# Performance work log

Hardware: AMD Instinct MI355X
Metric: run time of the kernel (lower is better)

## Reference

```python
import jax, jax.numpy as jnp
import numpy as np

B, L, D, H, FF = 2, 2048, 1024, 16, 4096


def _xavier(key, out_d, in_d):
    lim = (6.0 / (in_d + out_d)) ** 0.5
    return jax.random.uniform(key, (out_d, in_d), jnp.float32, -lim, lim)


def setup_inputs() -> dict:
    key = jax.random.key(0)
    ks = jax.random.split(key, 7)
    x = jax.random.normal(ks[0], (B, L, D), dtype=jnp.float32)
    wq = _xavier(ks[1], D, D)
    wk = _xavier(ks[2], D, D)
    wv = _xavier(ks[3], D, D)
    wo = _xavier(ks[4], D, D)
    w1 = _xavier(ks[5], FF, D)
    w2 = _xavier(ks[6], D, FF)
    zD = jnp.zeros((D,), jnp.float32)
    return dict(x=x, wq=wq, bq=zD, wk=wk, bk=zD, wv=wv, bv=zD, wo=wo, bo=zD,
                w1=w1, b1=jnp.zeros((FF,), jnp.float32), w2=w2, b2=zD)


def _ln2d(x, eps=1e-5):
    # F.layer_norm(x, x.shape[1:]): normalize jointly over (L, D), no affine
    mu = jnp.mean(x, axis=(1, 2), keepdims=True)
    var = jnp.var(x, axis=(1, 2), keepdims=True)
    return (x - mu) * jax.lax.rsqrt(var + eps)


def reference(x, wq, bq, wk, bk, wv, bv, wo, bo, w1, b1, w2, b2):
    Bx, Lx, Dx = x.shape
    nH = H
    Dh = Dx // nH
    h = _ln2d(x)
    q = (h @ wq.T + bq).reshape(Bx, Lx, nH, Dh).transpose(0, 2, 1, 3)  # (B,H,L,Dh)
    k = (h @ wk.T + bk).reshape(Bx, Lx, nH, Dh).transpose(0, 2, 1, 3)
    v = (h @ wv.T + bv).reshape(Bx, Lx, nH, Dh).transpose(0, 2, 1, 3)
    # NOTE: faithful to source bug: scale = 1/sqrt(key.size(dim=1)) = 1/sqrt(num_heads)
    scale = 1.0 / jnp.sqrt(jnp.asarray(nH, jnp.float32))
    att = jax.nn.softmax(jnp.einsum('bhqd,bhkd->bhqk', q, k) * scale, axis=-1)
    o = jnp.einsum('bhqk,bhkd->bhqd', att, v).transpose(0, 2, 1, 3).reshape(Bx, Lx, Dx)
    o = o @ wo.T + bo
    y = _ln2d(o + x)
    ff = jax.nn.relu(y @ w1.T + b1) @ w2.T + b2
    return ff + x  # second residual adds the ORIGINAL x (as in source)
```

## Files before the change

kernel.cpp:

```cpp
#include <hip/hip_runtime.h>
#include <cstdint>
#include <cstddef>

typedef unsigned short u16;
typedef unsigned int uint;
typedef __bf16 bf16x8 __attribute__((ext_vector_type(8)));
typedef float f32x4 __attribute__((ext_vector_type(4)));

#define BATCH 2
#define SEQ 2048
#define DIM 1024
#define NH 16
#define DH 64
#define FFD 4096
#define MROWS 4096
#define PER_BATCH 2097152

__device__ __forceinline__ u16 f2b(float f) {
  uint u = __builtin_bit_cast(uint, f);
  u += 0x7FFFu + ((u >> 16) & 1u);
  return (u16)(u >> 16);
}

__device__ __forceinline__ uint pkbf2(float a, float b) {
  u16 x = __builtin_bit_cast(u16, (__bf16)a);
  u16 y = __builtin_bit_cast(u16, (__bf16)b);
  return (uint)x | ((uint)y << 16);
}

__device__ __forceinline__ int xcd_swz(int flat, int nwg) {
  return (flat & 7) * (nwg >> 3) + (flat >> 3);
}

#define GLL(gp, lp)                                                            \
  __builtin_amdgcn_global_load_lds(                                            \
      (const __attribute__((address_space(1))) void*)(gp),                     \
      (__attribute__((address_space(3))) void*)(lp), 16, 0, 0)

__global__ __launch_bounds__(256) void cvt4_kernel(const float* __restrict__ s0,
                                                   const float* __restrict__ s1,
                                                   const float* __restrict__ s2,
                                                   const float* __restrict__ s3,
                                                   u16* d0, u16* d1, u16* d2, u16* d3,
                                                   int n) {
  int t = blockIdx.y;
  const float* src = (t == 0) ? s0 : (t == 1) ? s1 : (t == 2) ? s2 : s3;
  u16* dst = (t == 0) ? d0 : (t == 1) ? d1 : (t == 2) ? d2 : d3;
  int i = (blockIdx.x * 256 + threadIdx.x) * 8;
  if (i >= n) return;
  float4 a = *(const float4*)(src + i);
  float4 b = *(const float4*)(src + i + 4);
  uint4 o;
  o.x = f2b(a.x) | ((uint)f2b(a.y) << 16);
  o.y = f2b(a.z) | ((uint)f2b(a.w) << 16);
  o.z = f2b(b.x) | ((uint)f2b(b.y) << 16);
  o.w = f2b(b.z) | ((uint)f2b(b.w) << 16);
  *(uint4*)(dst + i) = o;
}

__global__ __launch_bounds__(256) void reduce_stats_kernel(const float* __restrict__ x,
                                                           float* __restrict__ stats) {
  int b = blockIdx.y;
  const float* p = x + (size_t)b * PER_BATCH;
  float s = 0.f, ss = 0.f;
  int stride = gridDim.x * 256 * 4;
  for (int i = (blockIdx.x * 256 + threadIdx.x) * 4; i < PER_BATCH; i += stride) {
    float4 v = *(const float4*)(p + i);
    s  += (v.x + v.y) + (v.z + v.w);
    ss += (v.x * v.x + v.y * v.y) + (v.z * v.z + v.w * v.w);
  }
#pragma unroll
  for (int m = 32; m; m >>= 1) { s += __shfl_xor(s, m); ss += __shfl_xor(ss, m); }
  __shared__ float red[16];
  int w = threadIdx.x >> 6;
  if ((threadIdx.x & 63) == 0) { red[w] = s; red[8 + w] = ss; }
  __syncthreads();
  if (threadIdx.x == 0) {
    atomicAdd(&stats[b * 2],     red[0] + red[1] + red[2] + red[3]);
    atomicAdd(&stats[b * 2 + 1], red[8] + red[9] + red[10] + red[11]);
  }
}

__global__ __launch_bounds__(256) void ln_apply_kernel(const float* __restrict__ xin,
                                                       const float* __restrict__ stats,
                                                       u16* __restrict__ out) {
  int i = (blockIdx.x * 256 + threadIdx.x) * 4;
  int b = i >> 21;
  const float inv = 1.f / (float)PER_BATCH;
  float mu = stats[b * 2] * inv;
  float var = stats[b * 2 + 1] * inv - mu * mu;
  float rs = rsqrtf(var + 1e-5f);
  float4 v = *(const float4*)(xin + i);
  uint r0 = f2b((v.x - mu) * rs) | ((uint)f2b((v.y - mu) * rs) << 16);
  uint r1 = f2b((v.z - mu) * rs) | ((uint)f2b((v.w - mu) * rs) << 16);
  *(uint2*)(out + i) = make_uint2(r0, r1);
}

template <int TN, int RELU, int RESID, int OUTBF, int TRV, int DBUF>
__device__ __forceinline__ void gemm_bt_body(const u16* __restrict__ A,
                                             const u16* __restrict__ Bm,
                                             const float* __restrict__ bias,
                                             const float* __restrict__ resid,
                                             void* __restrict__ Cout,
                                             int M, int N, int K,
                                             int m0, int n0, float oscale) {
  constexpr int AI  = (TN == 128) ? 4 : 2;
  constexpr int BCH = (TN == 128) ? 4 : 2;
  constexpr int NB  = DBUF ? 3 : 1;
  __shared__ __align__(16) u16 As[NB][128 * 64];
  __shared__ __align__(16) u16 Bs[NB][TN * 64];
  const int tid = threadIdx.x;
  const int lane = tid & 63, w = tid >> 6;
  const int wr = (TN == 128) ? (w >> 1) : w;
  const int wc = (TN == 128) ? (w & 1) : 0;
  const int ln = lane & 15, qd = lane >> 4;

  f32x4 acc[AI][4] = {};

  const int lrow = lane >> 3;
  const int scl  = (lane & 7) ^ lrow;
  const u16* Ag = A  + (size_t)(m0 + w * 32 + lrow) * K + scl * 8;
  const u16* Bg = Bm + (size_t)(n0 + w * 8 * BCH + lrow) * K + scl * 8;

  const int co0 = ((qd)     ^ (ln & 7)) * 8;
  const int co1 = ((4 + qd) ^ (ln & 7)) * 8;

  auto STAGE = [&](int buf, int k0) {
#pragma unroll
    for (int r = 0; r < 4; ++r)
      GLL(Ag + (size_t)(r * 8) * K + k0, As[buf] + (w * 4 + r) * 512);
#pragma unroll
    for (int r = 0; r < BCH; ++r)
      GLL(Bg + (size_t)(r * 8) * K + k0, Bs[buf] + (w * BCH + r) * 512);
  };

  auto COMPUTE = [&](int buf) {
#pragma unroll
    for (int kk = 0; kk < 2; ++kk) {
      const int co = kk ? co1 : co0;
      bf16x8 af[AI], bf[4];
#pragma unroll
      for (int t = 0; t < AI; ++t)
        af[t] = *(const bf16x8*)&As[buf][(wr * (AI * 16) + t * 16 + ln) * 64 + co];
#pragma unroll
      for (int t = 0; t < 4; ++t)
        bf[t] = *(const bf16x8*)&Bs[buf][(wc * 64 + t * 16 + ln) * 64 + co];
#pragma unroll
      for (int i = 0; i < AI; ++i)
#pragma unroll
        for (int j = 0; j < 4; ++j)
          acc[i][j] = __builtin_amdgcn_mfma_f32_16x16x32_bf16(af[i], bf[j], acc[i][j], 0, 0, 0);
    }
  };

  if constexpr (NB == 3) {
    const int nk = K >> 6;
    STAGE(0, 0);
    STAGE(1, 64);
    int c = 0, s = 2;
    int t = 0;
    for (; t + 1 < nk; ++t) {
      asm volatile("s_waitcnt vmcnt(6)" ::: "memory");
      __builtin_amdgcn_s_barrier();
      __builtin_amdgcn_sched_barrier(0);
      if (t + 2 < nk) STAGE(s, (t + 2) * 64);
      COMPUTE(c);
      c = (c == 2) ? 0 : c + 1;
      s = (s == 2) ? 0 : s + 1;
    }
    asm volatile("s_waitcnt vmcnt(0)" ::: "memory");
    __builtin_amdgcn_s_barrier();
    __builtin_amdgcn_sched_barrier(0);
    COMPUTE(c);
  } else {
    for (int k0 = 0; k0 < K; k0 += 64) {
      __syncthreads();
      STAGE(0, k0);
      __syncthreads();
      COMPUTE(0);
    }
  }

#pragma unroll
  for (int i = 0; i < AI; ++i) {
    int row = m0 + wr * (AI * 16) + i * 16 + qd * 4;
#pragma unroll
    for (int j = 0; j < 4; ++j) {
      int col = n0 + wc * 64 + j * 16 + ln;
      float bv = bias[col];
      if (TRV) {
        union { uint2 u2; u16 us[4]; } pk;
#pragma unroll
        for (int r = 0; r < 4; ++r) pk.us[r] = f2b(acc[i][j][r] + bv);
        *(uint2*)&((u16*)Cout)[(size_t)col * MROWS + row] = pk.u2;
      } else {
#pragma unroll
        for (int r = 0; r < 4; ++r) {
          float v = (acc[i][j][r] + bv) * oscale;
          if (RELU) v = fmaxf(v, 0.f);
          size_t off = (size_t)(row + r) * N + col;
          if (RESID) v += resid[off];
          if (OUTBF) ((u16*)Cout)[off] = f2b(v);
          else       ((float*)Cout)[off] = v;
        }
      }
    }
  }
}

template <int TN, int RELU, int RESID, int OUTBF, int DBUF>
__global__ __launch_bounds__(256) void gemm_bt_kernel(const u16* __restrict__ A,
                                                      const u16* __restrict__ Bm,
                                                      const float* __restrict__ bias,
                                                      const float* __restrict__ resid,
                                                      void* __restrict__ Cout,
                                                      int M, int N, int K) {
  const int nx = gridDim.x;
  const int nwg = nx * gridDim.y;
  const int wid = xcd_swz(blockIdx.x + nx * blockIdx.y, nwg);
  gemm_bt_body<TN, RELU, RESID, OUTBF, 0, DBUF>(A, Bm, bias, resid, Cout, M, N, K,
                                                (wid / nx) * 128, (wid % nx) * TN, 1.0f);
}

__global__ __launch_bounds__(256) void gemm_qkv_kernel(const u16* __restrict__ A,
                                                       const u16* B0, const u16* B1, const u16* B2,
                                                       const float* c0, const float* c1, const float* c2,
                                                       u16* o0, u16* o1, u16* o2) {
  int z = blockIdx.z;
  const int wid = xcd_swz(blockIdx.x + 8 * blockIdx.y, 256);
  const int m0 = (wid >> 3) * 128, n0 = (wid & 7) * 128;
  if (z == 2) {
    gemm_bt_body<128, 0, 0, 1, 1, 0>(A, B2, c2, nullptr, o2, MROWS, DIM, DIM,
                                     m0, n0, 1.0f);
  } else {
    const u16* Bm = (z == 0) ? B0 : B1;
    const float* bias = (z == 0) ? c0 : c1;
    u16* Cout = (z == 0) ? o0 : o1;
    float sc = (z == 0) ? 0.25f : 1.0f;
    gemm_bt_body<128, 0, 0, 1, 0, 0>(A, Bm, bias, nullptr, Cout, MROWS, DIM, DIM,
                                     m0, n0, sc);
  }
}

template <int RELU>
__global__ __launch_bounds__(512, 2) void gemm256_kernel(const u16* __restrict__ A,
                                                         const u16* __restrict__ Bm,
                                                         const float* __restrict__ bias,
                                                         u16* __restrict__ Cout,
                                                         int M, int N, int K) {
  __shared__ __align__(16) u16 As[2][256 * 64];
  __shared__ __align__(16) u16 Bs[2][256 * 64];
  const int tid = threadIdx.x;
  const int lane = tid & 63, w = tid >> 6;
  const int wr = w >> 2, wc = w & 3;
  const int ln = lane & 15, qd = lane >> 4;

  const int nx = gridDim.x;
  const int nwg = nx * gridDim.y;
  const int wid = xcd_swz(blockIdx.x + nx * blockIdx.y, nwg);
  const int m0 = (wid / nx) * 256, n0 = (wid % nx) * 256;

  f32x4 acc[8][4] = {};

  const int lrow = lane >> 3;
  const int scl  = (lane & 7) ^ lrow;
  const u16* Ag = A  + (size_t)(m0 + w * 32 + lrow) * K + scl * 8;
  const u16* Bg = Bm + (size_t)(n0 + w * 32 + lrow) * K + scl * 8;

  const int co0 = ((qd)     ^ (ln & 7)) * 8;
  const int co1 = ((4 + qd) ^ (ln & 7)) * 8;

  auto STAGE = [&](int buf, int k0) {
#pragma unroll
    for (int r = 0; r < 4; ++r) {
      GLL(Ag + (size_t)(r * 8) * K + k0, As[buf] + (w * 4 + r) * 512);
      GLL(Bg + (size_t)(r * 8) * K + k0, Bs[buf] + (w * 4 + r) * 512);
    }
  };

  auto COMPUTE = [&](int buf) {
#pragma unroll
    for (int kk = 0; kk < 2; ++kk) {
      const int co = kk ? co1 : co0;
      bf16x8 af[8], bf[4];
#pragma unroll
      for (int t = 0; t < 8; ++t)
        af[t] = *(const bf16x8*)&As[buf][(wr * 128 + t * 16 + ln) * 64 + co];
#pragma unroll
      for (int t = 0; t < 4; ++t)
        bf[t] = *(const bf16x8*)&Bs[buf][(wc * 64 + t * 16 + ln) * 64 + co];
      __builtin_amdgcn_s_setprio(1);
#pragma unroll
      for (int i = 0; i < 8; ++i)
#pragma unroll
        for (int j = 0; j < 4; ++j)
          acc[i][j] = __builtin_amdgcn_mfma_f32_16x16x32_bf16(af[i], bf[j], acc[i][j], 0, 0, 0);
      __builtin_amdgcn_s_setprio(0);
    }
  };

  const int nk = K >> 6;
  STAGE(0, 0);
  for (int t = 0; t < nk; ++t) {
    const int p = t & 1;
    __syncthreads();
    if (t + 1 < nk) STAGE(1 - p, (t + 1) * 64);
    COMPUTE(p);
  }

#pragma unroll
  for (int i = 0; i < 8; ++i) {
    int row = m0 + wr * 128 + i * 16 + qd * 4;
#pragma unroll
    for (int j = 0; j < 4; ++j) {
      int col = n0 + wc * 64 + j * 16 + ln;
      float bv = bias[col];
#pragma unroll
      for (int r = 0; r < 4; ++r) {
        float v = acc[i][j][r] + bv;
        if (RELU) v = fmaxf(v, 0.f);
        Cout[(size_t)(row + r) * N + col] = f2b(v);
      }
    }
  }
}

__global__ __launch_bounds__(256, 2) void attn_kernel(const u16* __restrict__ Q,
                                                      const u16* __restrict__ Km,
                                                      const u16* __restrict__ vT,
                                                      u16* __restrict__ O) {
  __shared__ __align__(16) u16 Ks[2][64 * 64];
  __shared__ __align__(16) u16 Vt[2][64 * 64];
  __shared__ __align__(16) u16 Ps[4][32 * 64];

  const int tid = threadIdx.x, lane = tid & 63, w = tid >> 6;
  const int ln = lane & 15, qd = lane >> 4;
  const int flat = blockIdx.x + 16 * (blockIdx.y + 16 * blockIdx.z);
  const int wid = xcd_swz(flat, 512);
  const int qi = wid & 15, head = (wid >> 4) & 15, b = wid >> 8;
  const int wq0 = b * SEQ + qi * 128 + w * 32;
  const int hcol = head * DH;

  bf16x8 qf[2][2];
#pragma unroll
  for (int ti = 0; ti < 2; ++ti)
#pragma unroll
    for (int kk = 0; kk < 2; ++kk)
      qf[ti][kk] = *(const bf16x8*)&Q[(size_t)(wq0 + ti * 16 + ln) * DIM + hcol + kk * 32 + qd * 8];

  union { u16 u[8]; bf16x8 v; } oneu;
#pragma unroll
  for (int e = 0; e < 8; ++e) oneu.u[e] = 0x3F80;
  const bf16x8 vones = oneu.v;

  f32x4 accO[2][4] = {};
  f32x4 accL[2] = {};

  const int srow = lane >> 3;
  const int scl  = (lane & 7) ^ srow;
  const u16* Kg = Km + (size_t)(b * SEQ + w * 16 + srow) * DIM + hcol + scl * 8;
  const u16* Vg = vT + (size_t)(hcol + w * 16 + srow) * MROWS + b * SEQ + scl * 8;
  u16* Pw = Ps[w];
  const int swz = ln & 7;

#pragma unroll
  for (int r = 0; r < 2; ++r) {
    GLL(Kg + (size_t)(r * 8) * DIM,   &Ks[0][(w * 2 + r) * 512]);
    GLL(Vg + (size_t)(r * 8) * MROWS, &Vt[0][(w * 2 + r) * 512]);
  }

  for (int t = 0; t < SEQ / 64; ++t) {
    const int p = t & 1;
    const int kt = t * 64;
    __syncthreads();

    if (t + 1 < SEQ / 64) {
      const int kt2 = kt + 64;
#pragma unroll
      for (int r = 0; r < 2; ++r) {
        GLL(Kg + (size_t)(kt2 + r * 8) * DIM,   &Ks[1 - p][(w * 2 + r) * 512]);
        GLL(Vg + (size_t)(r * 8) * MROWS + kt2, &Vt[1 - p][(w * 2 + r) * 512]);
      }
    }

    f32x4 sacc[4][2] = {};
#pragma unroll
    for (int kk = 0; kk < 2; ++kk) {
      bf16x8 kf[4];
#pragma unroll
      for (int tj = 0; tj < 4; ++tj)
        kf[tj] = *(const bf16x8*)&Ks[p][(tj * 16 + ln) * 64 + (((kk * 4 + qd) ^ swz) * 8)];
      __builtin_amdgcn_s_setprio(1);
#pragma unroll
      for (int tj = 0; tj < 4; ++tj)
#pragma unroll
        for (int ti = 0; ti < 2; ++ti)
          sacc[tj][ti] = __builtin_amdgcn_mfma_f32_16x16x32_bf16(kf[tj], qf[ti][kk], sacc[tj][ti], 0, 0, 0);
      __builtin_amdgcn_s_setprio(0);
    }

#pragma unroll
    for (int tj = 0; tj < 4; ++tj)
#pragma unroll
      for (int ti = 0; ti < 2; ++ti) {
        uint lo = pkbf2(__expf(sacc[tj][ti][0]), __expf(sacc[tj][ti][1]));
        uint hi = pkbf2(__expf(sacc[tj][ti][2]), __expf(sacc[tj][ti][3]));
        *(uint2*)&Pw[(ti * 16 + ln) * 64 + (((2 * tj + (qd >> 1)) ^ swz) * 8) + (qd & 1) * 4] =
            make_uint2(lo, hi);
      }

#pragma unroll
    for (int kk = 0; kk < 2; ++kk) {
      bf16x8 pf[2], vf[4];
#pragma unroll
      for (int ti = 0; ti < 2; ++ti)
        pf[ti] = *(const bf16x8*)&Pw[(ti * 16 + ln) * 64 + (((kk * 4 + qd) ^ swz) * 8)];
#pragma unroll
      for (int tjv = 0; tjv < 4; ++tjv)
        vf[tjv] = *(const bf16x8*)&Vt[p][(tjv * 16 + ln) * 64 + (((kk * 4 + qd) ^ swz) * 8)];
      __builtin_amdgcn_s_setprio(1);
#pragma unroll
      for (int ti = 0; ti < 2; ++ti) {
#pragma unroll
        for (int tjv = 0; tjv < 4; ++tjv)
          accO[ti][tjv] = __builtin_amdgcn_mfma_f32_16x16x32_bf16(pf[ti], vf[tjv], accO[ti][tjv], 0, 0, 0);
        accL[ti] = __builtin_amdgcn_mfma_f32_16x16x32_bf16(pf[ti], vones, accL[ti], 0, 0, 0);
      }
      __builtin_amdgcn_s_setprio(0);
    }
  }

#pragma unroll
  for (int ti = 0; ti < 2; ++ti)
#pragma unroll
    for (int r = 0; r < 4; ++r) {
      float inv = 1.f / accL[ti][r];
#pragma unroll
      for (int tjv = 0; tjv < 4; ++tjv)
        O[(size_t)(wq0 + ti * 16 + qd * 4 + r) * DIM + hcol + tjv * 16 + ln] =
            f2b(accO[ti][tjv][r] * inv);
    }
}

extern "C" void kernel_launch(void* const* d_in, const int* in_sizes, int n_in,
                              void* d_out, int out_size, void* d_ws, size_t ws_size,
                              hipStream_t stream) {
  const float* x  = (const float*)d_in[0];
  const float* wq = (const float*)d_in[1];
  const float* bq = (const float*)d_in[2];
  const float* wk = (const float*)d_in[3];
  const float* bk = (const float*)d_in[4];
  const float* wv = (const float*)d_in[5];
  const float* bv = (const float*)d_in[6];
  const float* wo = (const float*)d_in[7];
  const float* bo = (const float*)d_in[8];
  const float* w1 = (const float*)d_in[9];
  const float* b1 = (const float*)d_in[10];
  const float* w2 = (const float*)d_in[11];
  const float* b2 = (const float*)d_in[12];
  float* out = (float*)d_out;
  char* ws = (char*)d_ws;

  const size_t MB = 1u << 20;
  u16*   h    = (u16*)(ws + 0);
  u16*   q    = (u16*)(ws + 8  * MB);
  u16*   k    = (u16*)(ws + 16 * MB);
  u16*   v    = (u16*)(ws + 24 * MB);
  u16*   o    = (u16*)(ws + 32 * MB);
  u16*   r    = (u16*)(ws + 8  * MB);
  float* ares = (float*)(ws + 40 * MB);
  u16*   wqb  = (u16*)(ws + 56 * MB);
  u16*   wkb  = (u16*)(ws + 58 * MB);
  u16*   wvb  = (u16*)(ws + 60 * MB);
  u16*   wob  = (u16*)(ws + 62 * MB);
  u16*   w1b  = (u16*)(ws + 64 * MB);
  u16*   w2b  = (u16*)(ws + 72 * MB);
  float* stats= (float*)(ws + 80 * MB);
  u16*   y    = h;

  (void)hipMemsetAsync(stats, 0, 64, stream);

  cvt4_kernel<<<dim3(512, 4),  256, 0, stream>>>(wq, wk, wv, wo, wqb, wkb, wvb, wob, DIM * DIM);
  cvt4_kernel<<<dim3(2048, 2), 256, 0, stream>>>(w1, w2, w1, w2, w1b, w2b, w1b, w2b, FFD * DIM);

  reduce_stats_kernel<<<dim3(64, 2), 256, 0, stream>>>(x, stats);
  ln_apply_kernel<<<4096, 256, 0, stream>>>(x, stats, h);

  gemm_qkv_kernel<<<dim3(8, 32, 3), 256, 0, stream>>>(h, wqb, wkb, wvb, bq, bk, bv, q, k, v);

  attn_kernel<<<dim3(16, 16, 2), 256, 0, stream>>>(q, k, v, o);

  gemm_bt_kernel<64, 0, 1, 0, 1><<<dim3(16, 32), 256, 0, stream>>>(o, wob, bo, x, ares, MROWS, DIM, DIM);

  reduce_stats_kernel<<<dim3(64, 2), 256, 0, stream>>>(ares, stats + 4);
  ln_apply_kernel<<<4096, 256, 0, stream>>>(ares, stats + 4, y);

  gemm256_kernel<1><<<dim3(16, 16), 512, 0, stream>>>(y, w1b, b1, r, MROWS, FFD, DIM);

  gemm_bt_kernel<64, 0, 1, 0, 1><<<dim3(16, 32), 256, 0, stream>>>(r, w2b, b2, x, out, MROWS, DIM, FFD);
}
```

Before: 358.4 us.

## Shrink attention query tile to 64 rows per block and double grid

The attention kernel now gives each wave 16 query rows instead of 32, so a block covers 64 queries and the grid doubles to 1024 blocks. Launch bounds rise to 4 blocks per CU and the P scratch shrinks, cutting registers and shared memory per block to raise occupancy and spread work across more CUs. In exchange, each K/V tile loaded into shared memory now feeds half as many query rows, so total K/V traffic and load instructions per MFMA double.

After: 363.1 us. Within noise of the previous version (+1.3%).

```diff
diff --git a/kernel.cpp b/kernel.cpp
--- a/kernel.cpp
+++ b/kernel.cpp
@@ -325,36 +325,34 @@
   }
 }
 
-__global__ __launch_bounds__(256, 2) void attn_kernel(const u16* __restrict__ Q,
+__global__ __launch_bounds__(256, 4) void attn_kernel(const u16* __restrict__ Q,
                                                       const u16* __restrict__ Km,
                                                       const u16* __restrict__ vT,
                                                       u16* __restrict__ O) {
   __shared__ __align__(16) u16 Ks[2][64 * 64];
   __shared__ __align__(16) u16 Vt[2][64 * 64];
-  __shared__ __align__(16) u16 Ps[4][32 * 64];
+  __shared__ __align__(16) u16 Ps[4][16 * 64];
 
   const int tid = threadIdx.x, lane = tid & 63, w = tid >> 6;
   const int ln = lane & 15, qd = lane >> 4;
-  const int flat = blockIdx.x + 16 * (blockIdx.y + 16 * blockIdx.z);
-  const int wid = xcd_swz(flat, 512);
-  const int qi = wid & 15, head = (wid >> 4) & 15, b = wid >> 8;
-  const int wq0 = b * SEQ + qi * 128 + w * 32;
+  const int flat = blockIdx.x + 32 * (blockIdx.y + 16 * blockIdx.z);
+  const int wid = xcd_swz(flat, 1024);
+  const int qi = wid & 31, head = (wid >> 5) & 15, b = wid >> 9;
+  const int wq0 = b * SEQ + qi * 64 + w * 16;
   const int hcol = head * DH;
 
-  bf16x8 qf[2][2];
-#pragma unroll
-  for (int ti = 0; ti < 2; ++ti)
-#pragma unroll
-    for (int kk = 0; kk < 2; ++kk)
-      qf[ti][kk] = *(const bf16x8*)&Q[(size_t)(wq0 + ti * 16 + ln) * DIM + hcol + kk * 32 + qd * 8];
+  bf16x8 qf[2];
+#pragma unroll
+  for (int kk = 0; kk < 2; ++kk)
+    qf[kk] = *(const bf16x8*)&Q[(size_t)(wq0 + ln) * DIM + hcol + kk * 32 + qd * 8];
 
   union { u16 u[8]; bf16x8 v; } oneu;
 #pragma unroll
   for (int e = 0; e < 8; ++e) oneu.u[e] = 0x3F80;
   const bf16x8 vones = oneu.v;
 
-  f32x4 accO[2][4] = {};
-  f32x4 accL[2] = {};
+  f32x4 accO[4] = {};
+  f32x4 accL = {};
 
   const int srow = lane >> 3;
   const int scl  = (lane & 7) ^ srow;
@@ -383,7 +381,7 @@
       }
     }
 
-    f32x4 sacc[4][2] = {};
+    f32x4 sacc[4] = {};
 #pragma unroll
     for (int kk = 0; kk < 2; ++kk) {
       bf16x8 kf[4];
@@ -393,53 +391,42 @@
       __builtin_amdgcn_s_setprio(1);
 #pragma unroll
       for (int tj = 0; tj < 4; ++tj)
-#pragma unroll
-        for (int ti = 0; ti < 2; ++ti)
-          sacc[tj][ti] = __builtin_amdgcn_mfma_f32_16x16x32_bf16(kf[tj], qf[ti][kk], sacc[tj][ti], 0, 0, 0);
+        sacc[tj] = __builtin_amdgcn_mfma_f32_16x16x32_bf16(kf[tj], qf[kk], sacc[tj], 0, 0, 0);
       __builtin_amdgcn_s_setprio(0);
     }
 
 #pragma unroll
-    for (int tj = 0; tj < 4; ++tj)
-#pragma unroll
-      for (int ti = 0; ti < 2; ++ti) {
-        uint lo = pkbf2(__expf(sacc[tj][ti][0]), __expf(sacc[tj][ti][1]));
-        uint hi = pkbf2(__expf(sacc[tj][ti][2]), __expf(sacc[tj][ti][3]));
-        *(uint2*)&Pw[(ti * 16 + ln) * 64 + (((2 * tj + (qd >> 1)) ^ swz) * 8) + (qd & 1) * 4] =
-            make_uint2(lo, hi);
-      }
+    for (int tj = 0; tj < 4; ++tj) {
+      uint lo = pkbf2(__expf(sacc[tj][0]), __expf(sacc[tj][1]));
+      uint hi = pkbf2(__expf(sacc[tj][2]), __expf(sacc[tj][3]));
+      *(uint2*)&Pw[ln * 64 + (((2 * tj + (qd >> 1)) ^ swz) * 8) + (qd & 1) * 4] =
+          make_uint2(lo, hi);
+    }
 
 #pragma unroll
     for (int kk = 0; kk < 2; ++kk) {
-      bf16x8 pf[2], vf[4];
-#pragma unroll
-      for (int ti = 0; ti < 2; ++ti)
-        pf[ti] = *(const bf16x8*)&Pw[(ti * 16 + ln) * 64 + (((kk * 4 + qd) ^ swz) * 8)];
+      bf16x8 pf, vf[4];
+      pf = *(const bf16x8*)&Pw[ln * 64 + (((kk * 4 + qd) ^ swz) * 8)];
 #pragma unroll
       for (int tjv = 0; tjv < 4; ++tjv)
         vf[tjv] = *(const bf16x8*)&Vt[p][(tjv * 16 + ln) * 64 + (((kk * 4 + qd) ^ swz) * 8)];
       __builtin_amdgcn_s_setprio(1);
 #pragma unroll
-      for (int ti = 0; ti < 2; ++ti) {
-#pragma unroll
-        for (int tjv = 0; tjv < 4; ++tjv)
-          accO[ti][tjv] = __builtin_amdgcn_mfma_f32_16x16x32_bf16(pf[ti], vf[tjv], accO[ti][tjv], 0, 0, 0);
-        accL[ti] = __builtin_amdgcn_mfma_f32_16x16x32_bf16(pf[ti], vones, accL[ti], 0, 0, 0);
-      }
+      for (int tjv = 0; tjv < 4; ++tjv)
+        accO[tjv] = __builtin_amdgcn_mfma_f32_16x16x32_bf16(pf, vf[tjv], accO[tjv], 0, 0, 0);
+      accL = __builtin_amdgcn_mfma_f32_16x16x32_bf16(pf, vones, accL, 0, 0, 0);
       __builtin_amdgcn_s_setprio(0);
     }
   }
 
 #pragma unroll
-  for (int ti = 0; ti < 2; ++ti)
-#pragma unroll
-    for (int r = 0; r < 4; ++r) {
-      float inv = 1.f / accL[ti][r];
-#pragma unroll
-      for (int tjv = 0; tjv < 4; ++tjv)
-        O[(size_t)(wq0 + ti * 16 + qd * 4 + r) * DIM + hcol + tjv * 16 + ln] =
-            f2b(accO[ti][tjv][r] * inv);
-    }
+  for (int r = 0; r < 4; ++r) {
+    float inv = 1.f / accL[r];
+#pragma unroll
+    for (int tjv = 0; tjv < 4; ++tjv)
+      O[(size_t)(wq0 + qd * 4 + r) * DIM + hcol + tjv * 16 + ln] =
+          f2b(accO[tjv][r] * inv);
+  }
 }
 
 extern "C" void kernel_launch(void* const* d_in, const int* in_sizes, int n_in,
@@ -488,7 +475,7 @@
 
   gemm_qkv_kernel<<<dim3(8, 32, 3), 256, 0, stream>>>(h, wqb, wkb, wvb, bq, bk, bv, q, k, v);
 
-  attn_kernel<<<dim3(16, 16, 2), 256, 0, stream>>>(q, k, v, o);
+  attn_kernel<<<dim3(32, 16, 2), 256, 0, stream>>>(q, k, v, o);
 
   gemm_bt_kernel<64, 0, 1, 0, 1><<<dim3(16, 32), 256, 0, stream>>>(o, wob, bo, x, ares, MROWS, DIM, DIM);
 
```

## Fuse LayerNorm stats into out-proj GEMM epilogue; retile QKV GEMM to 128x64

Applied to the files above, without the earlier changes.

The output-projection GEMM epilogue now accumulates the per-batch sum and sum of squares of the residual output. It reduces them across the wavefront and adds them atomically to the stats buffer, so the separate reduce_stats kernel launch and its full re-read of the 16MB activation go away. Separately, the fused QKV GEMM switches from 128x128 single-buffered tiles to 128x64 triple-buffered tiles, doubling the grid to fill more CUs and overlap loads. The atomics add a small amount of contention, float summation order becomes nondeterministic, and narrower tiles reduce operand reuse in the QKV GEMM.

Result: slower. 426.3 us (+18.9%).

```diff
diff --git a/kernel.cpp b/kernel.cpp
--- a/kernel.cpp
+++ b/kernel.cpp
@@ -96,12 +96,13 @@
   *(uint2*)(out + i) = make_uint2(r0, r1);
 }
 
-template <int TN, int RELU, int RESID, int OUTBF, int TRV, int DBUF>
+template <int TN, int RELU, int RESID, int OUTBF, int TRV, int DBUF, int STATS>
 __device__ __forceinline__ void gemm_bt_body(const u16* __restrict__ A,
                                              const u16* __restrict__ Bm,
                                              const float* __restrict__ bias,
                                              const float* __restrict__ resid,
                                              void* __restrict__ Cout,
+                                             float* __restrict__ stats,
                                              int M, int N, int K,
                                              int m0, int n0, float oscale) {
   constexpr int AI  = (TN == 128) ? 4 : 2;
@@ -181,6 +182,8 @@
     }
   }
 
+  float sum = 0.f, ssum = 0.f;
+
 #pragma unroll
   for (int i = 0; i < AI; ++i) {
     int row = m0 + wr * (AI * 16) + i * 16 + qd * 4;
@@ -202,24 +205,37 @@
           if (RESID) v += resid[off];
           if (OUTBF) ((u16*)Cout)[off] = f2b(v);
           else       ((float*)Cout)[off] = v;
+          if (STATS) { sum += v; ssum += v * v; }
         }
       }
     }
   }
-}
-
-template <int TN, int RELU, int RESID, int OUTBF, int DBUF>
+
+  if (STATS) {
+#pragma unroll
+    for (int m = 32; m; m >>= 1) { sum += __shfl_xor(sum, m); ssum += __shfl_xor(ssum, m); }
+    if (lane == 0) {
+      int b = m0 >> 11;
+      atomicAdd(&stats[b * 2], sum);
+      atomicAdd(&stats[b * 2 + 1], ssum);
+    }
+  }
+}
+
+template <int TN, int RELU, int RESID, int OUTBF, int DBUF, int STATS>
 __global__ __launch_bounds__(256) void gemm_bt_kernel(const u16* __restrict__ A,
                                                       const u16* __restrict__ Bm,
                                                       const float* __restrict__ bias,
                                                       const float* __restrict__ resid,
                                                       void* __restrict__ Cout,
+                                                      float* __restrict__ stats,
                                                       int M, int N, int K) {
   const int nx = gridDim.x;
   const int nwg = nx * gridDim.y;
   const int wid = xcd_swz(blockIdx.x + nx * blockIdx.y, nwg);
-  gemm_bt_body<TN, RELU, RESID, OUTBF, 0, DBUF>(A, Bm, bias, resid, Cout, M, N, K,
-                                                (wid / nx) * 128, (wid % nx) * TN, 1.0f);
+  gemm_bt_body<TN, RELU, RESID, OUTBF, 0, DBUF, STATS>(A, Bm, bias, resid, Cout, stats,
+                                                       M, N, K,
+                                                       (wid / nx) * 128, (wid % nx) * TN, 1.0f);
 }
 
 __global__ __launch_bounds__(256) void gemm_qkv_kernel(const u16* __restrict__ A,
@@ -227,18 +243,18 @@
                                                        const float* c0, const float* c1, const float* c2,
                                                        u16* o0, u16* o1, u16* o2) {
   int z = blockIdx.z;
-  const int wid = xcd_swz(blockIdx.x + 8 * blockIdx.y, 256);
-  const int m0 = (wid >> 3) * 128, n0 = (wid & 7) * 128;
+  const int wid = xcd_swz(blockIdx.x + 16 * blockIdx.y, 512);
+  const int m0 = (wid >> 4) * 128, n0 = (wid & 15) * 64;
   if (z == 2) {
-    gemm_bt_body<128, 0, 0, 1, 1, 0>(A, B2, c2, nullptr, o2, MROWS, DIM, DIM,
-                                     m0, n0, 1.0f);
+    gemm_bt_body<64, 0, 0, 1, 1, 1, 0>(A, B2, c2, nullptr, o2, nullptr,
+                                       MROWS, DIM, DIM, m0, n0, 1.0f);
   } else {
     const u16* Bm = (z == 0) ? B0 : B1;
     const float* bias = (z == 0) ? c0 : c1;
     u16* Cout = (z == 0) ? o0 : o1;
     float sc = (z == 0) ? 0.25f : 1.0f;
-    gemm_bt_body<128, 0, 0, 1, 0, 0>(A, Bm, bias, nullptr, Cout, MROWS, DIM, DIM,
-                                     m0, n0, sc);
+    gemm_bt_body<64, 0, 0, 1, 0, 1, 0>(A, Bm, bias, nullptr, Cout, nullptr,
+                                       MROWS, DIM, DIM, m0, n0, sc);
   }
 }
 
@@ -486,16 +502,15 @@
   reduce_stats_kernel<<<dim3(64, 2), 256, 0, stream>>>(x, stats);
   ln_apply_kernel<<<4096, 256, 0, stream>>>(x, stats, h);
 
-  gemm_qkv_kernel<<<dim3(8, 32, 3), 256, 0, stream>>>(h, wqb, wkb, wvb, bq, bk, bv, q, k, v);
+  gemm_qkv_kernel<<<dim3(16, 32, 3), 256, 0, stream>>>(h, wqb, wkb, wvb, bq, bk, bv, q, k, v);
 
   attn_kernel<<<dim3(16, 16, 2), 256, 0, stream>>>(q, k, v, o);
 
-  gemm_bt_kernel<64, 0, 1, 0, 1><<<dim3(16, 32), 256, 0, stream>>>(o, wob, bo, x, ares, MROWS, DIM, DIM);
-
-  reduce_stats_kernel<<<dim3(64, 2), 256, 0, stream>>>(ares, stats + 4);
+  gemm_bt_kernel<64, 0, 1, 0, 1, 1><<<dim3(16, 32), 256, 0, stream>>>(o, wob, bo, x, ares, stats + 4, MROWS, DIM, DIM);
+
   ln_apply_kernel<<<4096, 256, 0, stream>>>(ares, stats + 4, y);
 
   gemm256_kernel<1><<<dim3(16, 16), 512, 0, stream>>>(y, w1b, b1, r, MROWS, FFD, DIM);
 
-  gemm_bt_kernel<64, 0, 1, 0, 1><<<dim3(16, 32), 256, 0, stream>>>(r, w2b, b2, x, out, MROWS, DIM, FFD);
-}
+  gemm_bt_kernel<64, 0, 1, 0, 1, 0><<<dim3(16, 32), 256, 0, stream>>>(r, w2b, b2, x, out, nullptr, MROWS, DIM, FFD);
+}
```
